# Kernel tuning notes

Hardware: AMD Instinct MI355X
Metric: run time of the kernel (lower is better)

## Reference

```python
import jax, jax.numpy as jnp
import numpy as np

D_MODEL = 1024
N_HEADS = 16
D_LATENT = 64
LN_EPS = 1e-5


def setup_inputs() -> dict:
    key = jax.random.key(0)
    ks = jax.random.split(key, 9)
    dm, h, dl = D_MODEL, N_HEADS, D_LATENT
    hd = h * dl
    # xavier_uniform with gain=0.1: limit = 0.1 * sqrt(6/(fan_in+fan_out))
    def xavier(k, fan_in, fan_out):
        lim = 0.1 * np.sqrt(6.0 / (fan_in + fan_out))
        return jax.random.uniform(k, (fan_in, fan_out), jnp.float32, -lim, lim)
    return {
        "x": jax.random.normal(ks[0], (4, 2048, dm), jnp.float32),
        "ln_g": jnp.ones((dm,), jnp.float32),
        "ln_b": jnp.zeros((dm,), jnp.float32),
        "wq": xavier(ks[1], dm, hd), "bq": jnp.zeros((hd,), jnp.float32),
        "wk": xavier(ks[2], dm, hd), "bk": jnp.zeros((hd,), jnp.float32),
        "wv": xavier(ks[3], dm, hd), "bv": jnp.zeros((hd,), jnp.float32),
        "wo": xavier(ks[4], hd, dm), "bo": jnp.zeros((dm,), jnp.float32),
    }


def reference(x, ln_g, ln_b, wq, bq, wk, bk, wv, bv, wo, bo):
    b, s, dm = x.shape
    h, dl = N_HEADS, D_LATENT
    # context = raw x (bound before LayerNorm in the torch code)
    context = x
    mu = jnp.mean(x, axis=-1, keepdims=True)
    var = jnp.var(x, axis=-1, keepdims=True)
    xn = (x - mu) * jax.lax.rsqrt(var + LN_EPS) * ln_g + ln_b
    q = (xn @ wq + bq).reshape(b, s, h, dl).transpose(0, 2, 1, 3)          # b h s d
    k = (context @ wk + bk).reshape(b, -1, h, dl).transpose(0, 2, 1, 3)    # b h t d
    v = (context @ wv + bv).reshape(b, -1, h, dl).transpose(0, 2, 1, 3)
    scores = jnp.einsum("bhsd,bhtd->bhst", q, k) / jnp.sqrt(jnp.float32(dl))
    attn = jax.nn.softmax(scores.astype(jnp.float32), axis=-1)
    # dropout omitted (eval mode / deterministic reference)
    out = jnp.einsum("bhst,bhtd->bhsd", attn, v)
    out = out.transpose(0, 2, 1, 3).reshape(b, s, h * dl)
    return out @ wo + bo
```

## Files before the change

kernel.cpp:

```cpp
#include <hip/hip_runtime.h>
#include <cstdint>

typedef __attribute__((ext_vector_type(8))) __bf16 bf16x8;
typedef __attribute__((ext_vector_type(8))) unsigned short u16x8;
typedef __attribute__((ext_vector_type(4))) unsigned short u16x4;
typedef __attribute__((ext_vector_type(4))) float f32x4;
typedef __attribute__((ext_vector_type(2))) unsigned int u32x2;
typedef __attribute__((ext_vector_type(4))) unsigned int u32x4;

__device__ inline unsigned short f2bf(float f) {
  return __builtin_bit_cast(unsigned short, (__bf16)f);
}

__device__ inline void llds16(const void* g, void* l) {
  __builtin_amdgcn_global_load_lds((const uint32_t*)g, (uint32_t*)l, 16, 0, 0);
}

__device__ inline bf16x8 ldfrag(const unsigned short* p) {
  u16x8 v = *(const u16x8*)p;
  return __builtin_bit_cast(bf16x8, v);
}

__device__ inline f32x4 mfma16(bf16x8 a, bf16x8 b, f32x4 c) {
  return __builtin_amdgcn_mfma_f32_16x16x32_bf16(a, b, c, 0, 0, 0);
}

__global__ __launch_bounds__(256) void ln_kernel(
    const float* __restrict__ x, const float* __restrict__ g, const float* __restrict__ be,
    unsigned short* __restrict__ xn, unsigned short* __restrict__ xb)
{
  const int row = blockIdx.x, tid = threadIdx.x;
  const size_t base = (size_t)row * 1024 + tid * 4;
  float4 v = *(const float4*)&x[base];
  float s  = v.x + v.y + v.z + v.w;
  float sq = v.x*v.x + v.y*v.y + v.z*v.z + v.w*v.w;
#pragma unroll
  for (int o = 1; o < 64; o <<= 1) { s += __shfl_xor(s, o); sq += __shfl_xor(sq, o); }
  __shared__ float ls[8];
  if ((tid & 63) == 0) { ls[tid >> 6] = s; ls[4 + (tid >> 6)] = sq; }
  __syncthreads();
  s  = ls[0] + ls[1] + ls[2] + ls[3];
  sq = ls[4] + ls[5] + ls[6] + ls[7];
  const float mu   = s * (1.f / 1024.f);
  const float var  = sq * (1.f / 1024.f) - mu * mu;
  const float rstd = rsqrtf(var + 1e-5f);
  float4 gv = *(const float4*)&g[tid * 4];
  float4 bv = *(const float4*)&be[tid * 4];
  u16x4 a, bb;
  a[0] = f2bf((v.x - mu) * rstd * gv.x + bv.x);
  a[1] = f2bf((v.y - mu) * rstd * gv.y + bv.y);
  a[2] = f2bf((v.z - mu) * rstd * gv.z + bv.z);
  a[3] = f2bf((v.w - mu) * rstd * gv.w + bv.w);
  bb[0] = f2bf(v.x); bb[1] = f2bf(v.y); bb[2] = f2bf(v.z); bb[3] = f2bf(v.w);
  *(u16x4*)&xn[base] = a;
  *(u16x4*)&xb[base] = bb;
}

__global__ __launch_bounds__(256) void wcast_kernel(
    const float* __restrict__ wq, const float* __restrict__ wk,
    const float* __restrict__ wv, const float* __restrict__ wo,
    unsigned short* __restrict__ wT, unsigned short* __restrict__ woT)
{
  __shared__ float t[64][66];
  const int z = blockIdx.z;
  const float* W = (z == 0) ? wq : (z == 1) ? wk : (z == 2) ? wv : wo;
  unsigned short* O = (z < 3) ? (wT + (size_t)z * 1048576) : woT;
  const int n0 = blockIdx.x * 64, k0 = blockIdx.y * 64;
  for (int idx = threadIdx.x; idx < 4096; idx += 256) {
    int r = idx >> 6, c = idx & 63;
    t[r][c] = W[(size_t)(k0 + r) * 1024 + n0 + c];
  }
  __syncthreads();
  for (int idx = threadIdx.x; idx < 4096; idx += 256) {
    int r = idx >> 6, c = idx & 63;
    O[(size_t)(n0 + r) * 1024 + k0 + c] = f2bf(t[c][r]);
  }
}

__global__ __launch_bounds__(512, 2) void gemm256_kernel(
    const unsigned short* __restrict__ A0, const unsigned short* __restrict__ A1,
    const unsigned short* __restrict__ BT,
    const float* __restrict__ b0, const float* __restrict__ b1, const float* __restrict__ b2,
    unsigned short* __restrict__ Cv, int M, int N, int K)
{
  __shared__ unsigned short S[65536];
  const int tid = threadIdx.x;
  const int wave = tid >> 6, lane = tid & 63;
  const int l15 = lane & 15, l4 = lane >> 4;
  const int swz = (l15 & 7) << 3;
  const int NBN = N >> 8;
  const int nwg = gridDim.x, cpx = nwg >> 3;
  const int orig = blockIdx.x;
  const int id = (orig & 7) * cpx + (orig >> 3);
  const int bn = id % NBN, bm = id / NBN;
  const int m0 = bm * 256, n0 = bn * 256;
  const unsigned short* Ap = (bn >= 4) ? A1 : A0;
  const int wr = (wave >> 2) * 128, wc = (wave & 3) * 64;

  f32x4 acc[8][4];
#pragma unroll
  for (int m = 0; m < 8; m++)
#pragma unroll
    for (int n = 0; n < 4; n++) acc[m][n] = {0.f, 0.f, 0.f, 0.f};

  auto ISSUE4 = [&](int b, int kt, int half) {
#pragma unroll
    for (int r = 0; r < 2; r++) {
      int rr = half * 2 + r;
      int D = tid * 16;
      int row = rr * 64 + (D >> 7);
      int colus = ((D & 127) >> 1) ^ ((row & 7) << 3);
      llds16(&Ap[(size_t)(m0 + row) * K + kt + colus],
             &S[b * 32768 + rr * 4096 + wave * 512]);
      llds16(&BT[(size_t)(n0 + row) * K + kt + colus],
             &S[b * 32768 + 16384 + rr * 4096 + wave * 512]);
    }
  };

  const int KSTEPS = K >> 6;
  ISSUE4(0, 0, 0); ISSUE4(0, 0, 1);
  for (int ki = 0; ki < KSTEPS; ki++) {
    const int cur = ki & 1;
    if (ki < KSTEPS - 1) {
      ISSUE4(cur ^ 1, (ki + 1) << 6, 0);
      asm volatile("s_waitcnt vmcnt(4)" ::: "memory");
    } else {
      asm volatile("s_waitcnt vmcnt(0)" ::: "memory");
    }
    __builtin_amdgcn_s_barrier();
    __builtin_amdgcn_sched_barrier(0);
    const unsigned short* Asb = &S[cur * 32768];
    const unsigned short* Bsb = &S[cur * 32768 + 16384];

    bf16x8 bf[4][2];
#pragma unroll
    for (int nf = 0; nf < 4; nf++)
#pragma unroll
      for (int ks = 0; ks < 2; ks++)
        bf[nf][ks] = ldfrag(&Bsb[(wc + nf * 16 + l15) * 64 + ((ks * 32 + l4 * 8) ^ swz)]);

#pragma unroll
    for (int ph = 0; ph < 2; ph++) {
      bf16x8 af[2][2];
#pragma unroll
      for (int i = 0; i < 2; i++)
#pragma unroll
        for (int ks = 0; ks < 2; ks++)
          af[i][ks] =
              ldfrag(&Asb[(wr + (ph * 2 + i) * 16 + l15) * 64 + ((ks * 32 + l4 * 8) ^ swz)]);
      __builtin_amdgcn_s_setprio(1);
#pragma unroll
      for (int ks = 0; ks < 2; ks++)
#pragma unroll
        for (int i = 0; i < 2; i++)
#pragma unroll
          for (int nf = 0; nf < 4; nf++)
            acc[ph * 2 + i][nf] = mfma16(af[i][ks], bf[nf][ks], acc[ph * 2 + i][nf]);
      __builtin_amdgcn_s_setprio(0);
    }

    if (ki < KSTEPS - 1) ISSUE4(cur ^ 1, (ki + 1) << 6, 1);

#pragma unroll
    for (int ph = 2; ph < 4; ph++) {
      bf16x8 af[2][2];
#pragma unroll
      for (int i = 0; i < 2; i++)
#pragma unroll
        for (int ks = 0; ks < 2; ks++)
          af[i][ks] =
              ldfrag(&Asb[(wr + (ph * 2 + i) * 16 + l15) * 64 + ((ks * 32 + l4 * 8) ^ swz)]);
      __builtin_amdgcn_s_setprio(1);
#pragma unroll
      for (int ks = 0; ks < 2; ks++)
#pragma unroll
        for (int i = 0; i < 2; i++)
#pragma unroll
          for (int nf = 0; nf < 4; nf++)
            acc[ph * 2 + i][nf] = mfma16(af[i][ks], bf[nf][ks], acc[ph * 2 + i][nf]);
      __builtin_amdgcn_s_setprio(0);
    }
    __builtin_amdgcn_s_barrier();
  }

#pragma unroll
  for (int nf = 0; nf < 4; nf++) {
    int c = n0 + wc + nf * 16 + l15;
    int sec = c >> 10;
    float bias = (sec == 0 ? b0 : (sec == 1 ? b1 : b2))[c & 1023];
    float sc = (sec == 0) ? 0.18033688011112042f : 1.0f;
    int h = (c >> 6) & 15, d = c & 63;
#pragma unroll
    for (int mf = 0; mf < 8; mf++) {
      int rbase = m0 + wr + mf * 16 + l4 * 4;
      int b = rbase >> 11, t = rbase & 2047;
      if (sec == 2) {
        u16x4 pk;
#pragma unroll
        for (int reg = 0; reg < 4; reg++) pk[reg] = f2bf(acc[mf][nf][reg] + bias);
        *(u16x4*)&Cv[(size_t)2 * 8388608 + ((size_t)((b * 16 + h) * 64 + d)) * 2048 + t] = pk;
      } else {
#pragma unroll
        for (int reg = 0; reg < 4; reg++) {
          float v = acc[mf][nf][reg] + bias;
          Cv[(size_t)sec * 8388608 + ((size_t)(b * 16 + h) * 2048 + t + reg) * 64 + d] =
              f2bf(v * sc);
        }
      }
    }
  }
}

template<int MODE>
__global__ __launch_bounds__(256) void gemm_kernel(
    const unsigned short* __restrict__ A0, const unsigned short* __restrict__ A1,
    const unsigned short* __restrict__ BT,
    const float* __restrict__ b0, const float* __restrict__ b1, const float* __restrict__ b2,
    void* __restrict__ Cv, int M, int N, int K)
{
  __shared__ unsigned short S[32768];
  const int tid = threadIdx.x;
  const int wave = tid >> 6, lane = tid & 63;
  const int l15 = lane & 15, l4 = lane >> 4;
  const int swz = (l15 & 7) << 3;
  const int NBN = N >> 7;
  const int nwg = gridDim.x, cpx = nwg >> 3;
  const int orig = blockIdx.x;
  const int id = (orig & 7) * cpx + (orig >> 3);
  const int bn = id % NBN, bm = id / NBN;
  const int m0 = bm * 128, n0 = bn * 128;
  const unsigned short* Ap = (MODE == 0 && bn >= 8) ? A1 : A0;
  const int wr = (wave >> 1) * 64, wc = (wave & 1) * 64;

  f32x4 acc[4][4];
#pragma unroll
  for (int m = 0; m < 4; m++)
#pragma unroll
    for (int n = 0; n < 4; n++) acc[m][n] = {0.f, 0.f, 0.f, 0.f};

  auto STAGE = [&](int b, int kt) {
#pragma unroll
    for (int r = 0; r < 4; r++) {
      int D = r * 4096 + tid * 16;
      int row = D >> 7;
      int colus = ((D & 127) >> 1) ^ ((row & 7) << 3);
      llds16(&Ap[(size_t)(m0 + row) * K + kt + colus], &S[b * 16384 + r * 2048 + wave * 512]);
      llds16(&BT[(size_t)(n0 + row) * K + kt + colus],
             &S[b * 16384 + 8192 + r * 2048 + wave * 512]);
    }
  };

  const int KSTEPS = K >> 6;
  int cur = 0;
  STAGE(0, 0);
  for (int ki = 0; ki < KSTEPS; ki++) {
    if (ki < KSTEPS - 1) {
      STAGE(cur ^ 1, (ki + 1) << 6);
      asm volatile("s_waitcnt vmcnt(8)" ::: "memory");
    } else {
      asm volatile("s_waitcnt vmcnt(0)" ::: "memory");
    }
    __builtin_amdgcn_s_barrier();
    __builtin_amdgcn_sched_barrier(0);
    const unsigned short* Asb = &S[cur * 16384];
    const unsigned short* Bsb = &S[cur * 16384 + 8192];
#pragma unroll
    for (int ks = 0; ks < 2; ks++) {
      bf16x8 af[4], bfr[4];
#pragma unroll
      for (int m = 0; m < 4; m++)
        af[m]  = ldfrag(&Asb[(wr + m * 16 + l15) * 64 + ((ks * 32 + l4 * 8) ^ swz)]);
#pragma unroll
      for (int n = 0; n < 4; n++)
        bfr[n] = ldfrag(&Bsb[(wc + n * 16 + l15) * 64 + ((ks * 32 + l4 * 8) ^ swz)]);
#pragma unroll
      for (int m = 0; m < 4; m++)
#pragma unroll
        for (int n = 0; n < 4; n++)
          acc[m][n] = mfma16(af[m], bfr[n], acc[m][n]);
    }
    __builtin_amdgcn_s_barrier();
    cur ^= 1;
  }

#pragma unroll
  for (int nf = 0; nf < 4; nf++) {
    int c = n0 + wc + nf * 16 + l15;
    if (MODE == 0) {
      int sec = c >> 10;
      float bias = (sec == 0 ? b0 : (sec == 1 ? b1 : b2))[c & 1023];
      float sc = (sec == 0) ? 0.18033688011112042f : 1.0f;
      int h = (c >> 6) & 15, d = c & 63;
#pragma unroll
      for (int mf = 0; mf < 4; mf++) {
        int rbase = m0 + wr + mf * 16 + l4 * 4;
        int b = rbase >> 11, t = rbase & 2047;
        if (sec == 2) {
          u16x4 pk;
#pragma unroll
          for (int reg = 0; reg < 4; reg++) pk[reg] = f2bf(acc[mf][nf][reg] + bias);
          *(u16x4*)&((unsigned short*)Cv)[(size_t)2 * 8388608 +
                                          ((size_t)((b * 16 + h) * 64 + d)) * 2048 + t] = pk;
        } else {
#pragma unroll
          for (int reg = 0; reg < 4; reg++) {
            float v = acc[mf][nf][reg] + bias;
            ((unsigned short*)Cv)[(size_t)sec * 8388608 +
                                  ((size_t)(b * 16 + h) * 2048 + t + reg) * 64 + d] =
                f2bf(v * sc);
          }
        }
      }
    } else {
      float bias = b0[c];
#pragma unroll
      for (int mf = 0; mf < 4; mf++) {
#pragma unroll
        for (int reg = 0; reg < 4; reg++) {
          int rrow = m0 + wr + mf * 16 + l4 * 4 + reg;
          ((float*)Cv)[(size_t)rrow * N + c] = acc[mf][nf][reg] + bias;
        }
      }
    }
  }
}

__global__ __launch_bounds__(512, 4) void attn_kernel(
    const unsigned short* __restrict__ Q,
    const unsigned short* __restrict__ Kg,
    const unsigned short* __restrict__ VTg,
    unsigned short* __restrict__ Oa)
{
  __shared__ unsigned short S[32768];
  const int tid = threadIdx.x;
  const int wave = tid >> 6, lane = tid & 63;
  const int l15 = lane & 15, l4 = lane >> 4;
  const int swz = (l15 & 7) << 3;
  const int orig = blockIdx.x;
  const int wg = ((orig & 7) << 6) + (orig >> 3);
  const int qb = wg & 7, bh = wg >> 3;
  const size_t bhbase = (size_t)bh * 131072;
  const int q0 = qb * 256 + wave * 32;

  const u16x8 onesu = {0x3F80, 0x3F80, 0x3F80, 0x3F80, 0x3F80, 0x3F80, 0x3F80, 0x3F80};
  const bf16x8 ones = __builtin_bit_cast(bf16x8, onesu);

  bf16x8 qf[2][2];
#pragma unroll
  for (int m = 0; m < 2; m++)
#pragma unroll
    for (int ks = 0; ks < 2; ks++)
      qf[m][ks] = ldfrag(&Q[bhbase + (size_t)(q0 + m * 16 + l15) * 64 + ks * 32 + l4 * 8]);

  f32x4 accO[2][4];
#pragma unroll
  for (int m = 0; m < 2; m++)
#pragma unroll
    for (int n = 0; n < 4; n++) accO[m][n] = {0.f, 0.f, 0.f, 0.f};
  f32x4 accR[2] = {{0.f, 0.f, 0.f, 0.f}, {0.f, 0.f, 0.f, 0.f}};

  auto STAGE = [&](int b, int jj) {
#pragma unroll
    for (int r = 0; r < 2; r++) {
      int D = r * 8192 + tid * 16;
      int rowK = D >> 7;
      int colKus = ((D & 127) >> 1) ^ ((rowK & 7) << 3);
      llds16(&Kg[bhbase + (size_t)(jj * 128 + rowK) * 64 + colKus],
             &S[b * 16384 + r * 4096 + wave * 512]);
      int rowV = D >> 8;
      int colVus = ((D & 255) >> 1) ^ ((rowV & 7) << 3);
      llds16(&VTg[bhbase + (size_t)rowV * 2048 + jj * 128 + colVus],
             &S[b * 16384 + 8192 + r * 4096 + wave * 512]);
    }
  };

  int cur = 0;
  STAGE(0, 0);
  for (int j = 0; j < 16; j++) {
    if (j < 15) {
      STAGE(cur ^ 1, j + 1);
      asm volatile("s_waitcnt vmcnt(4)" ::: "memory");
    } else {
      asm volatile("s_waitcnt vmcnt(0)" ::: "memory");
    }
    __builtin_amdgcn_s_barrier();
    __builtin_amdgcn_sched_barrier(0);

    const unsigned short* Kb = &S[cur * 16384];
    const unsigned short* Vb = &S[cur * 16384 + 8192];

#pragma unroll
    for (int kt = 0; kt < 4; kt++) {
      bf16x8 kf00 = ldfrag(&Kb[((2 * kt) * 16 + l15) * 64 + ((0 * 32 + l4 * 8) ^ swz)]);
      bf16x8 kf01 = ldfrag(&Kb[((2 * kt) * 16 + l15) * 64 + ((1 * 32 + l4 * 8) ^ swz)]);
      bf16x8 kf10 = ldfrag(&Kb[((2 * kt + 1) * 16 + l15) * 64 + ((0 * 32 + l4 * 8) ^ swz)]);
      bf16x8 kf11 = ldfrag(&Kb[((2 * kt + 1) * 16 + l15) * 64 + ((1 * 32 + l4 * 8) ^ swz)]);
      f32x4 sa = {0.f, 0.f, 0.f, 0.f}, sb = sa, sc = sa, sd = sa;
      __builtin_amdgcn_s_setprio(1);
      sa = mfma16(kf00, qf[0][0], sa); sb = mfma16(kf00, qf[1][0], sb);
      sc = mfma16(kf10, qf[0][0], sc); sd = mfma16(kf10, qf[1][0], sd);
      sa = mfma16(kf01, qf[0][1], sa); sb = mfma16(kf01, qf[1][1], sb);
      sc = mfma16(kf11, qf[0][1], sc); sd = mfma16(kf11, qf[1][1], sd);
      __builtin_amdgcn_s_setprio(0);

      bf16x8 vf[4];
#pragma unroll
      for (int n = 0; n < 4; n++)
        vf[n] = ldfrag(&Vb[(n * 16 + l15) * 128 + ((kt * 32 + l4 * 8) ^ swz)]);

      bf16x8 pf[2];
#pragma unroll
      for (int m = 0; m < 2; m++) {
        const f32x4 se = (m == 0) ? sa : sb;
        const f32x4 so = (m == 0) ? sc : sd;
        uint32_t V0, V1, V2, V3;
        {
          u16x4 pk;
#pragma unroll
          for (int r = 0; r < 4; r++) pk[r] = f2bf(__builtin_amdgcn_exp2f(se[r]));
          u32x2 w = __builtin_bit_cast(u32x2, pk);
          V0 = w[0]; V1 = w[1];
        }
        {
          u16x4 pk;
#pragma unroll
          for (int r = 0; r < 4; r++) pk[r] = f2bf(__builtin_amdgcn_exp2f(so[r]));
          u32x2 w = __builtin_bit_cast(u32x2, pk);
          V2 = w[0]; V3 = w[1];
        }
        asm("s_nop 1\n\t"
            "v_permlane32_swap_b32 %0, %2\n\t"
            "v_permlane32_swap_b32 %1, %3\n\t"
            "v_permlane16_swap_b32 %0, %2\n\t"
            "v_permlane16_swap_b32 %1, %3"
            : "+v"(V0), "+v"(V1), "+v"(V2), "+v"(V3));
        u32x4 fw = {V0, V1, V2, V3};
        pf[m] = __builtin_bit_cast(bf16x8, fw);
      }

      __builtin_amdgcn_s_setprio(1);
#pragma unroll
      for (int m = 0; m < 2; m++) {
        accR[m] = mfma16(pf[m], ones, accR[m]);
#pragma unroll
        for (int n = 0; n < 4; n++)
          accO[m][n] = mfma16(pf[m], vf[n], accO[m][n]);
      }
      __builtin_amdgcn_s_setprio(0);
    }

    __builtin_amdgcn_s_barrier();
    cur ^= 1;
  }

  const int b = bh >> 4, h = bh & 15;
#pragma unroll
  for (int m = 0; m < 2; m++)
#pragma unroll
    for (int reg = 0; reg < 4; reg++) {
      float inv = 1.0f / accR[m][reg];
      int srow = q0 + m * 16 + l4 * 4 + reg;
#pragma unroll
      for (int n = 0; n < 4; n++) {
        float v = accO[m][n][reg] * inv;
        Oa[((size_t)(b * 2048) + srow) * 1024 + h * 64 + n * 16 + l15] = f2bf(v);
      }
    }
}

extern "C" void kernel_launch(void* const* d_in, const int* in_sizes, int n_in,
                              void* d_out, int out_size, void* d_ws, size_t ws_size,
                              hipStream_t stream) {
  (void)in_sizes; (void)n_in; (void)out_size; (void)ws_size;
  const float* x   = (const float*)d_in[0];
  const float* lng = (const float*)d_in[1];
  const float* lnb = (const float*)d_in[2];
  const float* wq  = (const float*)d_in[3];
  const float* bq  = (const float*)d_in[4];
  const float* wk  = (const float*)d_in[5];
  const float* bk  = (const float*)d_in[6];
  const float* wv  = (const float*)d_in[7];
  const float* bv  = (const float*)d_in[8];
  const float* wo  = (const float*)d_in[9];
  const float* bo  = (const float*)d_in[10];

  unsigned short* ws = (unsigned short*)d_ws;
  const size_t NE = 8388608;
  unsigned short* xn  = ws;
  unsigned short* xb  = ws + NE;
  unsigned short* wT  = ws + 2 * NE;
  unsigned short* woT = wT + 3145728;
  unsigned short* qkv = woT + 1048576;
  unsigned short* oat = xb;

  wcast_kernel<<<dim3(16, 16, 4), 256, 0, stream>>>(wq, wk, wv, wo, wT, woT);
  ln_kernel<<<dim3(8192), 256, 0, stream>>>(x, lng, lnb, xn, xb);
  gemm256_kernel<<<dim3(384), 512, 0, stream>>>(xn, xb, wT, bq, bk, bv, qkv, 8192, 3072, 1024);
  attn_kernel<<<dim3(512), 512, 0, stream>>>(qkv, qkv + NE, qkv + 2 * NE, oat);
  gemm_kernel<1><<<dim3(512), 256, 0, stream>>>(oat, oat, woT, bo, bo, bo, d_out, 8192, 1024, 1024);
}
```

Measured before the change: 186.2 us.

## Restructure QKV GEMM main loop into four barrier-separated phases with interleaved prefetch

Reorganizes the K-loop of the fused QKV projection GEMM into four phases, each loading one k-slice's B fragments and four A fragments into registers. The prefetch of the next tile's global-to-LDS loads is split across the first two phases, and a barrier follows each phase. The vmcnt(0) wait is moved to the end of the iteration instead of the start. The aim is to cut live fragment registers and interleave memory issue with MFMA work more evenly, in the style of ping-pong scheduling. The cost is two barriers per phase, eight per K step, which adds synchronization overhead.

```diff
diff --git a/kernel.cpp b/kernel.cpp
--- a/kernel.cpp
+++ b/kernel.cpp
@@ -103,84 +103,58 @@
 #pragma unroll
     for (int n = 0; n < 4; n++) acc[m][n] = {0.f, 0.f, 0.f, 0.f};
 
-  auto ISSUE4 = [&](int b, int kt, int half) {
-#pragma unroll
-    for (int r = 0; r < 2; r++) {
-      int rr = half * 2 + r;
-      int D = tid * 16;
-      int row = rr * 64 + (D >> 7);
-      int colus = ((D & 127) >> 1) ^ ((row & 7) << 3);
-      llds16(&Ap[(size_t)(m0 + row) * K + kt + colus],
-             &S[b * 32768 + rr * 4096 + wave * 512]);
-      llds16(&BT[(size_t)(n0 + row) * K + kt + colus],
-             &S[b * 32768 + 16384 + rr * 4096 + wave * 512]);
-    }
+  auto ISSUE2 = [&](int b, int kt, int r) {
+    int D = tid * 16;
+    int row = r * 64 + (D >> 7);
+    int colus = ((D & 127) >> 1) ^ ((row & 7) << 3);
+    llds16(&Ap[(size_t)(m0 + row) * K + kt + colus], &S[b * 32768 + r * 4096 + wave * 512]);
+    llds16(&BT[(size_t)(n0 + row) * K + kt + colus],
+           &S[b * 32768 + 16384 + r * 4096 + wave * 512]);
   };
 
   const int KSTEPS = K >> 6;
-  ISSUE4(0, 0, 0); ISSUE4(0, 0, 1);
+  ISSUE2(0, 0, 0); ISSUE2(0, 0, 1); ISSUE2(0, 0, 2); ISSUE2(0, 0, 3);
+  asm volatile("s_waitcnt vmcnt(0)" ::: "memory");
+  __builtin_amdgcn_s_barrier();
+
   for (int ki = 0; ki < KSTEPS; ki++) {
     const int cur = ki & 1;
-    if (ki < KSTEPS - 1) {
-      ISSUE4(cur ^ 1, (ki + 1) << 6, 0);
-      asm volatile("s_waitcnt vmcnt(4)" ::: "memory");
-    } else {
-      asm volatile("s_waitcnt vmcnt(0)" ::: "memory");
-    }
-    __builtin_amdgcn_s_barrier();
-    __builtin_amdgcn_sched_barrier(0);
+    const int nk = (ki + 1) << 6;
+    const bool pre = ki < KSTEPS - 1;
     const unsigned short* Asb = &S[cur * 32768];
     const unsigned short* Bsb = &S[cur * 32768 + 16384];
-
-    bf16x8 bf[4][2];
-#pragma unroll
-    for (int nf = 0; nf < 4; nf++)
-#pragma unroll
-      for (int ks = 0; ks < 2; ks++)
-        bf[nf][ks] = ldfrag(&Bsb[(wc + nf * 16 + l15) * 64 + ((ks * 32 + l4 * 8) ^ swz)]);
-
-#pragma unroll
-    for (int ph = 0; ph < 2; ph++) {
-      bf16x8 af[2][2];
-#pragma unroll
-      for (int i = 0; i < 2; i++)
-#pragma unroll
-        for (int ks = 0; ks < 2; ks++)
-          af[i][ks] =
-              ldfrag(&Asb[(wr + (ph * 2 + i) * 16 + l15) * 64 + ((ks * 32 + l4 * 8) ^ swz)]);
+    bf16x8 bfr[4], af[4];
+
+#pragma unroll
+    for (int ph = 0; ph < 4; ph++) {
+      const int ks = ph >> 1;
+      const int mh = (ph & 1) * 4;
+      if (!(ph & 1)) {
+#pragma unroll
+        for (int nf = 0; nf < 4; nf++)
+          bfr[nf] = ldfrag(&Bsb[(wc + nf * 16 + l15) * 64 + ((ks * 32 + l4 * 8) ^ swz)]);
+      }
+#pragma unroll
+      for (int i = 0; i < 4; i++)
+        af[i] = ldfrag(&Asb[(wr + (mh + i) * 16 + l15) * 64 + ((ks * 32 + l4 * 8) ^ swz)]);
+      if (pre && ph < 2) {
+        ISSUE2(cur ^ 1, nk, ph * 2);
+        ISSUE2(cur ^ 1, nk, ph * 2 + 1);
+      }
+      __builtin_amdgcn_s_barrier();
+      __builtin_amdgcn_sched_barrier(0);
       __builtin_amdgcn_s_setprio(1);
 #pragma unroll
-      for (int ks = 0; ks < 2; ks++)
-#pragma unroll
-        for (int i = 0; i < 2; i++)
-#pragma unroll
-          for (int nf = 0; nf < 4; nf++)
-            acc[ph * 2 + i][nf] = mfma16(af[i][ks], bf[nf][ks], acc[ph * 2 + i][nf]);
+      for (int i = 0; i < 4; i++)
+#pragma unroll
+        for (int nf = 0; nf < 4; nf++)
+          acc[mh + i][nf] = mfma16(af[i], bfr[nf], acc[mh + i][nf]);
       __builtin_amdgcn_s_setprio(0);
-    }
-
-    if (ki < KSTEPS - 1) ISSUE4(cur ^ 1, (ki + 1) << 6, 1);
-
-#pragma unroll
-    for (int ph = 2; ph < 4; ph++) {
-      bf16x8 af[2][2];
-#pragma unroll
-      for (int i = 0; i < 2; i++)
-#pragma unroll
-        for (int ks = 0; ks < 2; ks++)
-          af[i][ks] =
-              ldfrag(&Asb[(wr + (ph * 2 + i) * 16 + l15) * 64 + ((ks * 32 + l4 * 8) ^ swz)]);
-      __builtin_amdgcn_s_setprio(1);
-#pragma unroll
-      for (int ks = 0; ks < 2; ks++)
-#pragma unroll
-        for (int i = 0; i < 2; i++)
-#pragma unroll
-          for (int nf = 0; nf < 4; nf++)
-            acc[ph * 2 + i][nf] = mfma16(af[i][ks], bf[nf][ks], acc[ph * 2 + i][nf]);
-      __builtin_amdgcn_s_setprio(0);
-    }
-    __builtin_amdgcn_s_barrier();
+      if (ph == 3)
+        asm volatile("s_waitcnt vmcnt(0)" ::: "memory");
+      __builtin_amdgcn_s_barrier();
+      __builtin_amdgcn_sched_barrier(0);
+    }
   }
 
 #pragma unroll
```

Measured after the change: 187.8 us. No clear change (+0.8%).
